# Optimization experiments

Measured on AMD Instinct MI355X. Metric: run time of the kernel, lower is better.

Reference implementation:

```python
import jax, jax.numpy as jnp
import numpy as np

B, S, D_IN, D_OUT = 4, 2048, 2048, 2048
EPS = 1e-10


def setup_inputs() -> dict:
    key = jax.random.key(0)
    kx, kw, kb = jax.random.split(key, 3)
    x = jax.random.normal(kx, (B, S, D_IN), dtype=jnp.float32)
    weight = jax.random.normal(kw, (D_OUT, D_IN), dtype=jnp.float32) * 0.02
    bias = jax.random.normal(kb, (D_OUT,), dtype=jnp.float32) * 0.02
    return {"x": x, "weight": weight, "bias": bias}


def reference(x, weight, bias):
    # abs-mean scale over the whole weight matrix (scalar)
    scale = jnp.mean(jnp.abs(weight))
    # ternary quantization: round(w/scale) clamped to {-1, 0, 1}
    w_t = jnp.clip(jnp.round(weight / (scale + EPS)), -1.0, 1.0)
    # straight-through estimator: forward uses w_t*scale, grad flows to weight
    w_ste = weight + jax.lax.stop_gradient(w_t * scale - weight)
    # F.linear: x @ w_ste.T + bias
    return jnp.einsum('bsi,oi->bso', x, w_ste) + bias
```

## Files before the change

### kernel.cpp

```cpp
#include <hip/hip_runtime.h>
#include <hip/hip_bf16.h>
#include <stdint.h>

#define M_DIM 8192
#define N_DIM 2048
#define K_DIM 2048
#define NT    (K_DIM / 64)

typedef float f32x4 __attribute__((ext_vector_type(4)));
typedef short bf16x8 __attribute__((ext_vector_type(8)));

typedef const __attribute__((address_space(1))) char* gp_t;
typedef __attribute__((address_space(3))) char* lp_t;

static __device__ __forceinline__ void gload_lds16(const void* g, void* l) {
  __builtin_amdgcn_global_load_lds((gp_t)(uintptr_t)g, (lp_t)(uint32_t)(uintptr_t)l, 16, 0, 0);
}

static __device__ __forceinline__ unsigned short f2bf(float f) {
  unsigned int u = __float_as_uint(f);
  unsigned int r = (u + 0x7FFFu + ((u >> 16) & 1u)) >> 16;
  return (unsigned short)r;
}

__global__ void cvt_x_absum(const float* __restrict__ x, unsigned short* __restrict__ xb,
                            const float* __restrict__ w, float* __restrict__ partials) {
  const int b = blockIdx.x;
  if (b < 16384) {
    int tid = b * 256 + threadIdx.x;
    float4 v = ((const float4*)x)[tid];
    ushort4 o;
    o.x = f2bf(v.x); o.y = f2bf(v.y); o.z = f2bf(v.z); o.w = f2bf(v.w);
    ((ushort4*)xb)[tid] = o;
  } else {
    int tid = (b - 16384) * 256 + threadIdx.x;
    const float4* w4 = (const float4*)w;
    float s = 0.f;
#pragma unroll
    for (int i = 0; i < 4; ++i) {
      float4 v = w4[tid + i * 262144];
      s += fabsf(v.x) + fabsf(v.y) + fabsf(v.z) + fabsf(v.w);
    }
#pragma unroll
    for (int off = 32; off > 0; off >>= 1) s += __shfl_down(s, off, 64);
    __shared__ float ls[4];
    if ((threadIdx.x & 63) == 0) ls[threadIdx.x >> 6] = s;
    __syncthreads();
    if (threadIdx.x == 0) partials[b - 16384] = (ls[0] + ls[1]) + (ls[2] + ls[3]);
  }
}

__global__ void quant_w(const float* __restrict__ w, const float* __restrict__ partials,
                        unsigned short* __restrict__ wt, float* __restrict__ scale_out) {
  __shared__ float ls[4];
  float s = 0.f;
#pragma unroll
  for (int i = 0; i < 4; ++i) s += partials[threadIdx.x + i * 256];
#pragma unroll
  for (int off = 32; off > 0; off >>= 1) s += __shfl_down(s, off, 64);
  if ((threadIdx.x & 63) == 0) ls[threadIdx.x >> 6] = s;
  __syncthreads();
  const float scale = ((ls[0] + ls[1]) + (ls[2] + ls[3])) * (1.0f / 4194304.0f);
  if (blockIdx.x == 0 && threadIdx.x == 0) scale_out[0] = scale;

  const float inv = 1.0f / (scale + 1e-10f);
  int tid = blockIdx.x * 256 + threadIdx.x;
  float4 v = ((const float4*)w)[tid];
  ushort4 o;
  float t;
  t = fminf(1.f, fmaxf(-1.f, rintf(v.x * inv))); o.x = f2bf(t);
  t = fminf(1.f, fmaxf(-1.f, rintf(v.y * inv))); o.y = f2bf(t);
  t = fminf(1.f, fmaxf(-1.f, rintf(v.z * inv))); o.z = f2bf(t);
  t = fminf(1.f, fmaxf(-1.f, rintf(v.w * inv))); o.w = f2bf(t);
  ((ushort4*)wt)[tid] = o;
}


#define VMCNT(n) asm volatile("s_waitcnt vmcnt(" #n ")" ::: "memory")
#define FENCE    asm volatile("" ::: "memory")
#define BARRIER  do { FENCE; __builtin_amdgcn_s_barrier(); FENCE; } while (0)

#define READ_A_TO(mh, dst)                                                                      \
  do {                                                                                          \
    _Pragma("unroll") for (int i = 0; i < 4; ++i) {                                             \
      dst[i][0] = *(const bf16x8*)(curA + (wr * 128 + (mh) * 64 + i * 16) * 128 + rd0);         \
      dst[i][1] = *(const bf16x8*)(curA + (wr * 128 + (mh) * 64 + i * 16) * 128 + rd1);         \
    }                                                                                           \
  } while (0)

#define READ_B_TO(nh, dst)                                                                      \
  do {                                                                                          \
    _Pragma("unroll") for (int j = 0; j < 2; ++j) {                                             \
      dst[j][0] = *(const bf16x8*)(curB + (wc * 64 + (nh) * 32 + j * 16) * 128 + rd0);          \
      dst[j][1] = *(const bf16x8*)(curB + (wc * 64 + (nh) * 32 + j * 16) * 128 + rd1);          \
    }                                                                                           \
  } while (0)

#define MFMA_Q(mh, nh, ar, br)                                                                  \
  do {                                                                                          \
    __builtin_amdgcn_s_setprio(1);                                                              \
    _Pragma("unroll") for (int i = 0; i < 4; ++i)                                               \
      _Pragma("unroll") for (int j = 0; j < 2; ++j)                                             \
        acc[(mh) * 4 + i][(nh) * 2 + j] = __builtin_amdgcn_mfma_f32_16x16x32_bf16(              \
            ar[i][0], br[j][0], acc[(mh) * 4 + i][(nh) * 2 + j], 0, 0, 0);                      \
    _Pragma("unroll") for (int i = 0; i < 4; ++i)                                               \
      _Pragma("unroll") for (int j = 0; j < 2; ++j)                                             \
        acc[(mh) * 4 + i][(nh) * 2 + j] = __builtin_amdgcn_mfma_f32_16x16x32_bf16(              \
            ar[i][1], br[j][1], acc[(mh) * 4 + i][(nh) * 2 + j], 0, 0, 0);                      \
    __builtin_amdgcn_s_setprio(0);                                                              \
  } while (0)

#define SA(bufsel, r) gload_lds16(Ag + offA[r] + ktA, ldsb + (bufsel) * 65536 + tid * 16 + (r) * 8192)
#define SB(bufsel, r) gload_lds16(Bg + offB[r] + ktB, ldsb + (bufsel) * 65536 + 32768 + tid * 16 + (r) * 8192)

__global__ void __launch_bounds__(512, 2)
gemm_bt(const unsigned short* __restrict__ A, const unsigned short* __restrict__ Bt,
        const float* __restrict__ bias, const float* __restrict__ scale_p,
        float* __restrict__ out) {
  __shared__ __align__(16) char lds_raw[131072];
  char* ldsb = (char*)lds_raw;

  const int tid = threadIdx.x;
  const int lane = tid & 63;
  const int wid = tid >> 6;
  const int wr = wid >> 2;
  const int wc = wid & 3;
  const int l15 = lane & 15, lhi = lane >> 4;

  const int swzl = (l15 & 7) << 4;
  const int rd0 = l15 * 128 + ((lhi * 16) ^ swzl);
  const int rd1 = l15 * 128 + (((lhi * 16) ^ 64) ^ swzl);

  const int bid = blockIdx.x;
  const int swz = (bid & 7) * 32 + (bid >> 3);
  const int bm = swz >> 3;
  const int bn = swz & 7;
  const int m0 = bm << 8, n0 = bn << 8;

  const int srow = tid >> 3;
  const int scol = (((tid & 7) ^ ((tid >> 3) & 7)) << 4);
  const char* Ag = (const char*)A;
  const char* Bg = (const char*)Bt;
  uint32_t offA[4], offB[4];
#pragma unroll
  for (int r = 0; r < 4; ++r) {
    offA[r] = (uint32_t)(m0 + srow + r * 64) * (K_DIM * 2) + scol;
    offB[r] = (uint32_t)(n0 + srow + r * 64) * (K_DIM * 2) + scol;
  }
  uint32_t ktA = 0, ktB = 0;

  f32x4 acc[8][4];
#pragma unroll
  for (int m = 0; m < 8; ++m)
#pragma unroll
    for (int n = 0; n < 4; ++n) {
      f32x4 z = {0.f, 0.f, 0.f, 0.f};
      acc[m][n] = z;
    }

  SA(0, 0); SA(0, 1); SA(0, 2); SA(0, 3);
  SB(0, 0); SB(0, 1); SB(0, 2); SB(0, 3);
  ktB = 128;
  SB(1, 0); SB(1, 1); SB(1, 2); SB(1, 3);
  ktA = 128; ktB = 256;
  VMCNT(4);
  BARRIER;

  bf16x8 a0[4][2], a1[4][2], b0[2][2], b1[2][2];

  for (int t = 0; t < NT; ++t) {
    const int cb = t & 1;
    const char* curA = ldsb + cb * 65536;
    const char* curB = curA + 32768;

    READ_A_TO(0, a0);
    READ_B_TO(0, b0);
    READ_B_TO(1, b1);
    READ_A_TO(1, a1);
    if (t < NT - 1) { SA(cb ^ 1, 0); SA(cb ^ 1, 1); SA(cb ^ 1, 2); SA(cb ^ 1, 3); ktA += 128; }

    MFMA_Q(0, 0, a0, b0);
    MFMA_Q(0, 1, a0, b1);

    BARRIER;

    if (t < NT - 2) { SB(cb, 0); SB(cb, 1); SB(cb, 2); SB(cb, 3); ktB += 128; }
    MFMA_Q(1, 0, a1, b0);
    MFMA_Q(1, 1, a1, b1);

    if (t < NT - 2) {
      VMCNT(4);
    } else {
      VMCNT(0);
    }
    BARRIER;
  }

  const float scale = scale_p[0];
#pragma unroll
  for (int n = 0; n < 4; ++n) {
    const int col = n0 + wc * 64 + n * 16 + l15;
    const float bv = bias[col];
#pragma unroll
    for (int m = 0; m < 8; ++m) {
      const int r0 = m0 + wr * 128 + m * 16 + lhi * 4;
      float* op = out + (size_t)r0 * N_DIM + col;
#pragma unroll
      for (int j = 0; j < 4; ++j) op[(size_t)j * N_DIM] = acc[m][n][j] * scale + bv;
    }
  }
}

extern "C" void kernel_launch(void* const* d_in, const int* in_sizes, int n_in,
                              void* d_out, int out_size, void* d_ws, size_t ws_size,
                              hipStream_t stream) {
  (void)in_sizes; (void)n_in; (void)out_size; (void)ws_size;
  const float* x    = (const float*)d_in[0];
  const float* w    = (const float*)d_in[1];
  const float* bias = (const float*)d_in[2];
  float* out = (float*)d_out;

  float* partials = (float*)d_ws;
  float* scale_slot = partials + 1024;
  unsigned short* wt = (unsigned short*)((char*)d_ws + 8192);
  unsigned short* xb = (unsigned short*)((char*)d_ws + 8192 + (size_t)N_DIM * K_DIM * 2);

  cvt_x_absum<<<17408, 256, 0, stream>>>(x, xb, w, partials);
  quant_w<<<4096, 256, 0, stream>>>(w, partials, wt, scale_slot);
  gemm_bt<<<256, 512, 0, stream>>>(xb, wt, bias, scale_slot, out);
}
```

Before: 84.60 us.

## Fuse fp32-to-bf16 conversion of X into GEMM A-tile loading

Drops the separate pass that converted X to bf16 in workspace. The GEMM now loads fp32 X tiles into registers, converts them to bf16 and writes them into swizzled LDS, with a new pipeline: register prefetch of the next A tile, direct-to-LDS loads for B, and one full vmcnt/lgkmcnt wait plus barrier per K step. This removes a write and re-read of a 32MB intermediate, but doubles A-side global traffic per tile (each A tile is re-read by 8 column blocks) and uses more registers and less asynchronous overlap.

```diff
diff --git a/kernel.cpp b/kernel.cpp
--- a/kernel.cpp
+++ b/kernel.cpp
@@ -23,31 +23,21 @@
   return (unsigned short)r;
 }
 
-__global__ void cvt_x_absum(const float* __restrict__ x, unsigned short* __restrict__ xb,
-                            const float* __restrict__ w, float* __restrict__ partials) {
-  const int b = blockIdx.x;
-  if (b < 16384) {
-    int tid = b * 256 + threadIdx.x;
-    float4 v = ((const float4*)x)[tid];
-    ushort4 o;
-    o.x = f2bf(v.x); o.y = f2bf(v.y); o.z = f2bf(v.z); o.w = f2bf(v.w);
-    ((ushort4*)xb)[tid] = o;
-  } else {
-    int tid = (b - 16384) * 256 + threadIdx.x;
-    const float4* w4 = (const float4*)w;
-    float s = 0.f;
-#pragma unroll
-    for (int i = 0; i < 4; ++i) {
-      float4 v = w4[tid + i * 262144];
-      s += fabsf(v.x) + fabsf(v.y) + fabsf(v.z) + fabsf(v.w);
-    }
-#pragma unroll
-    for (int off = 32; off > 0; off >>= 1) s += __shfl_down(s, off, 64);
-    __shared__ float ls[4];
-    if ((threadIdx.x & 63) == 0) ls[threadIdx.x >> 6] = s;
-    __syncthreads();
-    if (threadIdx.x == 0) partials[b - 16384] = (ls[0] + ls[1]) + (ls[2] + ls[3]);
-  }
+__global__ void absum_partials(const float* __restrict__ w, float* __restrict__ partials) {
+  int tid = blockIdx.x * 256 + threadIdx.x;
+  const float4* w4 = (const float4*)w;
+  float s = 0.f;
+#pragma unroll
+  for (int i = 0; i < 4; ++i) {
+    float4 v = w4[tid + i * 262144];
+    s += fabsf(v.x) + fabsf(v.y) + fabsf(v.z) + fabsf(v.w);
+  }
+#pragma unroll
+  for (int off = 32; off > 0; off >>= 1) s += __shfl_down(s, off, 64);
+  __shared__ float ls[4];
+  if ((threadIdx.x & 63) == 0) ls[threadIdx.x >> 6] = s;
+  __syncthreads();
+  if (threadIdx.x == 0) partials[blockIdx.x] = (ls[0] + ls[1]) + (ls[2] + ls[3]);
 }
 
 __global__ void quant_w(const float* __restrict__ w, const float* __restrict__ partials,
@@ -77,6 +67,7 @@
 
 
 #define VMCNT(n) asm volatile("s_waitcnt vmcnt(" #n ")" ::: "memory")
+#define LGKM0    asm volatile("s_waitcnt lgkmcnt(0)" ::: "memory")
 #define FENCE    asm volatile("" ::: "memory")
 #define BARRIER  do { FENCE; __builtin_amdgcn_s_barrier(); FENCE; } while (0)
 
@@ -110,11 +101,28 @@
     __builtin_amdgcn_s_setprio(0);                                                              \
   } while (0)
 
-#define SA(bufsel, r) gload_lds16(Ag + offA[r] + ktA, ldsb + (bufsel) * 65536 + tid * 16 + (r) * 8192)
+#define LOAD_A_REGS()                                                                           \
+  do {                                                                                          \
+    _Pragma("unroll") for (int r = 0; r < 4; ++r) {                                             \
+      av[2 * r]     = *(const float4*)(Xg + gofA[r] + ktA);                                     \
+      av[2 * r + 1] = *(const float4*)(Xg + gofA[r] + ktA + 16);                                \
+    }                                                                                           \
+  } while (0)
+
+#define CVT_WRITE_A(bufsel, r)                                                                  \
+  do {                                                                                          \
+    bf16x8 wv;                                                                                  \
+    wv[0] = (short)f2bf(av[2 * r].x);     wv[1] = (short)f2bf(av[2 * r].y);                     \
+    wv[2] = (short)f2bf(av[2 * r].z);     wv[3] = (short)f2bf(av[2 * r].w);                     \
+    wv[4] = (short)f2bf(av[2 * r + 1].x); wv[5] = (short)f2bf(av[2 * r + 1].y);                 \
+    wv[6] = (short)f2bf(av[2 * r + 1].z); wv[7] = (short)f2bf(av[2 * r + 1].w);                 \
+    *(bf16x8*)(ldsb + (bufsel) * 65536 + awr_off[r]) = wv;                                      \
+  } while (0)
+
 #define SB(bufsel, r) gload_lds16(Bg + offB[r] + ktB, ldsb + (bufsel) * 65536 + 32768 + tid * 16 + (r) * 8192)
 
 __global__ void __launch_bounds__(512, 2)
-gemm_bt(const unsigned short* __restrict__ A, const unsigned short* __restrict__ Bt,
+gemm_bt(const float* __restrict__ X, const unsigned short* __restrict__ Bt,
         const float* __restrict__ bias, const float* __restrict__ scale_p,
         float* __restrict__ out) {
   __shared__ __align__(16) char lds_raw[131072];
@@ -137,16 +145,23 @@
   const int bn = swz & 7;
   const int m0 = bm << 8, n0 = bn << 8;
 
-  const int srow = tid >> 3;
+  const int arow = tid >> 3;
+  const int acol = (tid & 7) << 4;
+  uint32_t gofA[4], awr_off[4];
+#pragma unroll
+  for (int r = 0; r < 4; ++r) {
+    gofA[r] = (uint32_t)(m0 + arow + r * 64) * (K_DIM * 4) + (acol << 1);
+    const int row_r = arow + r * 64;
+    awr_off[r] = (uint32_t)(row_r * 128 + (acol ^ ((row_r & 7) << 4)));
+  }
   const int scol = (((tid & 7) ^ ((tid >> 3) & 7)) << 4);
-  const char* Ag = (const char*)A;
+  const char* Xg = (const char*)X;
   const char* Bg = (const char*)Bt;
-  uint32_t offA[4], offB[4];
-#pragma unroll
-  for (int r = 0; r < 4; ++r) {
-    offA[r] = (uint32_t)(m0 + srow + r * 64) * (K_DIM * 2) + scol;
-    offB[r] = (uint32_t)(n0 + srow + r * 64) * (K_DIM * 2) + scol;
-  }
+  uint32_t offB[4];
+#pragma unroll
+  for (int r = 0; r < 4; ++r)
+    offB[r] = (uint32_t)(n0 + arow + r * 64) * (K_DIM * 2) + scol;
+
   uint32_t ktA = 0, ktB = 0;
 
   f32x4 acc[8][4];
@@ -158,12 +173,14 @@
       acc[m][n] = z;
     }
 
-  SA(0, 0); SA(0, 1); SA(0, 2); SA(0, 3);
+  float4 av[8];
+
+  LOAD_A_REGS();
   SB(0, 0); SB(0, 1); SB(0, 2); SB(0, 3);
-  ktB = 128;
-  SB(1, 0); SB(1, 1); SB(1, 2); SB(1, 3);
-  ktA = 128; ktB = 256;
-  VMCNT(4);
+  CVT_WRITE_A(0, 0); CVT_WRITE_A(0, 1); CVT_WRITE_A(0, 2); CVT_WRITE_A(0, 3);
+  ktA = 256; ktB = 128;
+  VMCNT(0);
+  LGKM0;
   BARRIER;
 
   bf16x8 a0[4][2], a1[4][2], b0[2][2], b1[2][2];
@@ -173,26 +190,25 @@
     const char* curA = ldsb + cb * 65536;
     const char* curB = curA + 32768;
 
+    if (t < NT - 1) {
+      LOAD_A_REGS();
+      SB(cb ^ 1, 0); SB(cb ^ 1, 1); SB(cb ^ 1, 2); SB(cb ^ 1, 3);
+    }
+
     READ_A_TO(0, a0);
     READ_B_TO(0, b0);
     READ_B_TO(1, b1);
     READ_A_TO(1, a1);
-    if (t < NT - 1) { SA(cb ^ 1, 0); SA(cb ^ 1, 1); SA(cb ^ 1, 2); SA(cb ^ 1, 3); ktA += 128; }
 
     MFMA_Q(0, 0, a0, b0);
+    if (t < NT - 1) { CVT_WRITE_A(cb ^ 1, 0); CVT_WRITE_A(cb ^ 1, 1); }
     MFMA_Q(0, 1, a0, b1);
-
-    BARRIER;
-
-    if (t < NT - 2) { SB(cb, 0); SB(cb, 1); SB(cb, 2); SB(cb, 3); ktB += 128; }
+    if (t < NT - 1) { CVT_WRITE_A(cb ^ 1, 2); CVT_WRITE_A(cb ^ 1, 3); ktA += 256; ktB += 128; }
     MFMA_Q(1, 0, a1, b0);
     MFMA_Q(1, 1, a1, b1);
 
-    if (t < NT - 2) {
-      VMCNT(4);
-    } else {
-      VMCNT(0);
-    }
+    VMCNT(0);
+    LGKM0;
     BARRIER;
   }
 
@@ -221,11 +237,10 @@
   float* out = (float*)d_out;
 
   float* partials = (float*)d_ws;
-  float* scale_slot = partials + 1024;
+  float* scale_slot = (float*)((char*)d_ws + 4096);
   unsigned short* wt = (unsigned short*)((char*)d_ws + 8192);
-  unsigned short* xb = (unsigned short*)((char*)d_ws + 8192 + (size_t)N_DIM * K_DIM * 2);
-
-  cvt_x_absum<<<17408, 256, 0, stream>>>(x, xb, w, partials);
+
+  absum_partials<<<1024, 256, 0, stream>>>(w, partials);
   quant_w<<<4096, 256, 0, stream>>>(w, partials, wt, scale_slot);
-  gemm_bt<<<256, 512, 0, stream>>>(xb, wt, bias, scale_slot, out);
-}
+  gemm_bt<<<256, 512, 0, stream>>>(x, wt, bias, scale_slot, out);
+}
```

New measurement: 117.7 us. 1.39x slower.

## Switch GEMM to BK=32 tiles with four-stage LDS ring buffer

Applied to the files above, without the earlier changes.

Halves the K-tile depth to 32 and replaces the split A/B double-buffer schedule with a four-buffer ring that keeps three tiles of global-to-LDS loads in flight. Each iteration issues the next stage's loads, reads all fragments, runs 32 MFMAs, then waits and barriers once. The LDS swizzle and staging offsets are changed to match the 64-byte rows. The aim is deeper prefetch to hide memory latency. The cost is twice as many barriers and loop iterations, and LDS reads of only 64 bytes per row.

```diff
diff --git a/kernel.cpp b/kernel.cpp
--- a/kernel.cpp
+++ b/kernel.cpp
@@ -5,7 +5,7 @@
 #define M_DIM 8192
 #define N_DIM 2048
 #define K_DIM 2048
-#define NT    (K_DIM / 64)
+#define NT    (K_DIM / 32)
 
 typedef float f32x4 __attribute__((ext_vector_type(4)));
 typedef short bf16x8 __attribute__((ext_vector_type(8)));
@@ -80,38 +80,27 @@
 #define FENCE    asm volatile("" ::: "memory")
 #define BARRIER  do { FENCE; __builtin_amdgcn_s_barrier(); FENCE; } while (0)
 
-#define READ_A_TO(mh, dst)                                                                      \
+#define SA(bufsel, r) gload_lds16(Ag + offA[r] + ktA, ldsb + (bufsel) * 32768 + tid * 16 + (r) * 8192)
+#define SB(bufsel, r) gload_lds16(Bg + offB[r] + ktB, ldsb + (bufsel) * 32768 + 16384 + tid * 16 + (r) * 8192)
+
+#define TILE_BODY(CB, STG, DO_STAGE, VM)                                                        \
   do {                                                                                          \
-    _Pragma("unroll") for (int i = 0; i < 4; ++i) {                                             \
-      dst[i][0] = *(const bf16x8*)(curA + (wr * 128 + (mh) * 64 + i * 16) * 128 + rd0);         \
-      dst[i][1] = *(const bf16x8*)(curA + (wr * 128 + (mh) * 64 + i * 16) * 128 + rd1);         \
-    }                                                                                           \
+    const char* base = ldsb + (CB) * 32768;                                                     \
+    bf16x8 af[8], bfr[4];                                                                       \
+    if (DO_STAGE) { SA(STG, 0); SA(STG, 1); SB(STG, 0); SB(STG, 1); ktA += 64; ktB += 64; }     \
+    _Pragma("unroll") for (int fr = 0; fr < 8; ++fr)                                            \
+      af[fr] = *(const bf16x8*)(base + wr * 8192 + fr * 1024 + rdoff);                          \
+    _Pragma("unroll") for (int fn = 0; fn < 4; ++fn)                                            \
+      bfr[fn] = *(const bf16x8*)(base + 16384 + wc * 4096 + fn * 1024 + rdoff);                 \
+    __builtin_amdgcn_s_setprio(1);                                                              \
+    _Pragma("unroll") for (int fr = 0; fr < 8; ++fr)                                            \
+      _Pragma("unroll") for (int fn = 0; fn < 4; ++fn)                                          \
+        acc[fr][fn] = __builtin_amdgcn_mfma_f32_16x16x32_bf16(af[fr], bfr[fn],                  \
+                                                              acc[fr][fn], 0, 0, 0);           \
+    __builtin_amdgcn_s_setprio(0);                                                              \
+    VM;                                                                                         \
+    BARRIER;                                                                                    \
   } while (0)
-
-#define READ_B_TO(nh, dst)                                                                      \
-  do {                                                                                          \
-    _Pragma("unroll") for (int j = 0; j < 2; ++j) {                                             \
-      dst[j][0] = *(const bf16x8*)(curB + (wc * 64 + (nh) * 32 + j * 16) * 128 + rd0);          \
-      dst[j][1] = *(const bf16x8*)(curB + (wc * 64 + (nh) * 32 + j * 16) * 128 + rd1);          \
-    }                                                                                           \
-  } while (0)
-
-#define MFMA_Q(mh, nh, ar, br)                                                                  \
-  do {                                                                                          \
-    __builtin_amdgcn_s_setprio(1);                                                              \
-    _Pragma("unroll") for (int i = 0; i < 4; ++i)                                               \
-      _Pragma("unroll") for (int j = 0; j < 2; ++j)                                             \
-        acc[(mh) * 4 + i][(nh) * 2 + j] = __builtin_amdgcn_mfma_f32_16x16x32_bf16(              \
-            ar[i][0], br[j][0], acc[(mh) * 4 + i][(nh) * 2 + j], 0, 0, 0);                      \
-    _Pragma("unroll") for (int i = 0; i < 4; ++i)                                               \
-      _Pragma("unroll") for (int j = 0; j < 2; ++j)                                             \
-        acc[(mh) * 4 + i][(nh) * 2 + j] = __builtin_amdgcn_mfma_f32_16x16x32_bf16(              \
-            ar[i][1], br[j][1], acc[(mh) * 4 + i][(nh) * 2 + j], 0, 0, 0);                      \
-    __builtin_amdgcn_s_setprio(0);                                                              \
-  } while (0)
-
-#define SA(bufsel, r) gload_lds16(Ag + offA[r] + ktA, ldsb + (bufsel) * 65536 + tid * 16 + (r) * 8192)
-#define SB(bufsel, r) gload_lds16(Bg + offB[r] + ktB, ldsb + (bufsel) * 65536 + 32768 + tid * 16 + (r) * 8192)
 
 __global__ void __launch_bounds__(512, 2)
 gemm_bt(const unsigned short* __restrict__ A, const unsigned short* __restrict__ Bt,
@@ -127,9 +116,7 @@
   const int wc = wid & 3;
   const int l15 = lane & 15, lhi = lane >> 4;
 
-  const int swzl = (l15 & 7) << 4;
-  const int rd0 = l15 * 128 + ((lhi * 16) ^ swzl);
-  const int rd1 = l15 * 128 + (((lhi * 16) ^ 64) ^ swzl);
+  const int rdoff = l15 * 64 + ((lhi * 16) ^ ((l15 & 3) << 4));
 
   const int bid = blockIdx.x;
   const int swz = (bid & 7) * 32 + (bid >> 3);
@@ -137,15 +124,15 @@
   const int bn = swz & 7;
   const int m0 = bm << 8, n0 = bn << 8;
 
-  const int srow = tid >> 3;
-  const int scol = (((tid & 7) ^ ((tid >> 3) & 7)) << 4);
+  const int srow = tid >> 2;
+  const int scol = (((tid & 3) ^ ((tid >> 2) & 3)) << 4);
   const char* Ag = (const char*)A;
   const char* Bg = (const char*)Bt;
-  uint32_t offA[4], offB[4];
-#pragma unroll
-  for (int r = 0; r < 4; ++r) {
-    offA[r] = (uint32_t)(m0 + srow + r * 64) * (K_DIM * 2) + scol;
-    offB[r] = (uint32_t)(n0 + srow + r * 64) * (K_DIM * 2) + scol;
+  uint32_t offA[2], offB[2];
+#pragma unroll
+  for (int r = 0; r < 2; ++r) {
+    offA[r] = (uint32_t)(m0 + srow + r * 128) * (K_DIM * 2) + scol;
+    offB[r] = (uint32_t)(n0 + srow + r * 128) * (K_DIM * 2) + scol;
   }
   uint32_t ktA = 0, ktB = 0;
 
@@ -158,41 +145,41 @@
       acc[m][n] = z;
     }
 
-  SA(0, 0); SA(0, 1); SA(0, 2); SA(0, 3);
-  SB(0, 0); SB(0, 1); SB(0, 2); SB(0, 3);
-  ktB = 128;
-  SB(1, 0); SB(1, 1); SB(1, 2); SB(1, 3);
-  ktA = 128; ktB = 256;
-  VMCNT(4);
+  SA(0, 0); SA(0, 1); SB(0, 0); SB(0, 1); ktA = 64;  ktB = 64;
+  SA(1, 0); SA(1, 1); SB(1, 0); SB(1, 1); ktA = 128; ktB = 128;
+  SA(2, 0); SA(2, 1); SB(2, 0); SB(2, 1); ktA = 192; ktB = 192;
+  VMCNT(8);
   BARRIER;
 
-  bf16x8 a0[4][2], a1[4][2], b0[2][2], b1[2][2];
-
-  for (int t = 0; t < NT; ++t) {
-    const int cb = t & 1;
-    const char* curA = ldsb + cb * 65536;
-    const char* curB = curA + 32768;
-
-    READ_A_TO(0, a0);
-    READ_B_TO(0, b0);
-    READ_B_TO(1, b1);
-    READ_A_TO(1, a1);
-    if (t < NT - 1) { SA(cb ^ 1, 0); SA(cb ^ 1, 1); SA(cb ^ 1, 2); SA(cb ^ 1, 3); ktA += 128; }
-
-    MFMA_Q(0, 0, a0, b0);
-    MFMA_Q(0, 1, a0, b1);
-
-    BARRIER;
-
-    if (t < NT - 2) { SB(cb, 0); SB(cb, 1); SB(cb, 2); SB(cb, 3); ktB += 128; }
-    MFMA_Q(1, 0, a1, b0);
-    MFMA_Q(1, 1, a1, b1);
-
-    if (t < NT - 2) {
-      VMCNT(4);
-    } else {
-      VMCNT(0);
-    }
+  for (int it = 0; it < 14; ++it) {
+    TILE_BODY(0, 3, 1, VMCNT(8));
+    TILE_BODY(1, 0, 1, VMCNT(8));
+    TILE_BODY(2, 1, 1, VMCNT(8));
+    TILE_BODY(3, 2, 1, VMCNT(8));
+  }
+
+  for (int t = 56; t < NT; ++t) {
+    const int cb = t & 3;
+    const int stg = (t + 3) & 3;
+    const char* base = ldsb + cb * 32768;
+    bf16x8 af[8], bfr[4];
+    if (t <= NT - 4) { SA(stg, 0); SA(stg, 1); SB(stg, 0); SB(stg, 1); ktA += 64; ktB += 64; }
+#pragma unroll
+    for (int fr = 0; fr < 8; ++fr)
+      af[fr] = *(const bf16x8*)(base + wr * 8192 + fr * 1024 + rdoff);
+#pragma unroll
+    for (int fn = 0; fn < 4; ++fn)
+      bfr[fn] = *(const bf16x8*)(base + 16384 + wc * 4096 + fn * 1024 + rdoff);
+    __builtin_amdgcn_s_setprio(1);
+#pragma unroll
+    for (int fr = 0; fr < 8; ++fr)
+#pragma unroll
+      for (int fn = 0; fn < 4; ++fn)
+        acc[fr][fn] = __builtin_amdgcn_mfma_f32_16x16x32_bf16(af[fr], bfr[fn], acc[fr][fn], 0, 0, 0);
+    __builtin_amdgcn_s_setprio(0);
+    if (t <= NT - 4) { VMCNT(8); }
+    else if (t == NT - 3) { VMCNT(4); }
+    else { VMCNT(0); }
     BARRIER;
   }
 
```

Result: slower. 94.19 us (+11.3%).
